# Performance work log

Hardware: AMD Instinct MI355X
Metric: run time of the kernel (lower is better)

The kernel has to match this reference:

```python
import jax, jax.numpy as jnp
import numpy as np

ANCHORS = jnp.array([[116.0, 90.0], [156.0, 198.0], [373.0, 326.0]], dtype=jnp.float32)
NUM_CLASSES = 80
IMG_SIZE = 416
EXP_CLAMP = 1000.0


def setup_inputs() -> dict:
    key = jax.random.key(0)
    # (batch, num_anchor*(num_classes+5), G, G) = (64, 255, 52, 52)
    X = jax.random.normal(key, (64, 255, 52, 52), dtype=jnp.float32)
    return {"X": X}


def reference(X):
    B = X.shape[0]
    G = X.shape[2]
    A = ANCHORS.shape[0]
    C = NUM_CLASSES
    ratio = IMG_SIZE / G  # stride

    # (B, A, 5+C, G, G) -> (B, A, G, G, 5+C)
    pred = X.reshape(B, A, C + 5, G, G).transpose(0, 1, 3, 4, 2)

    x = jax.nn.sigmoid(pred[..., 0])
    y = jax.nn.sigmoid(pred[..., 1])
    w = pred[..., 2]
    h = pred[..., 3]
    conf = jax.nn.sigmoid(pred[..., 4])
    clss = pred[..., 5:]  # raw logits, matching the torch module

    grid = jnp.arange(G, dtype=jnp.float32)
    coor_x = grid.reshape(1, 1, 1, G)   # varies along last (column) axis
    coor_y = grid.reshape(1, 1, G, 1)   # varies along row axis

    scale_anchors = ANCHORS / ratio
    anchor_x = scale_anchors[:, 0].reshape(1, A, 1, 1)
    anchor_y = scale_anchors[:, 1].reshape(1, A, 1, 1)

    bx = x + coor_x
    by = y + coor_y
    bw = jnp.minimum(jnp.exp(w), EXP_CLAMP) * anchor_x
    bh = jnp.minimum(jnp.exp(h), EXP_CLAMP) * anchor_y
    pred_boxes = jnp.stack([bx, by, bw, bh], axis=-1)  # (B, A, G, G, 4)

    output = jnp.concatenate(
        [
            pred_boxes.reshape(B, -1, 4) * ratio,
            conf.reshape(B, -1, 1),
            clss.reshape(B, -1, C),
        ],
        axis=-1,
    )  # (B, A*G*G, 5+C)
    return output
```

## Files before the change

kernel.cpp:

```cpp
#include <hip/hip_runtime.h>
#include <math.h>


constexpr int G   = 52;
constexpr int GG  = G * G;
constexpr int NA  = 3;
constexpr int NC  = 85;
constexpr int RPW = 16;
constexpr int WTB = GG / RPW;
constexpr float RATIO = 8.0f;

typedef float f32x4 __attribute__((ext_vector_type(4)));

__device__ __forceinline__ float sigmoidf_(float v) {
    return 1.0f / (1.0f + expf(-v));
}

__global__ __launch_bounds__(256)
void yolo_head_kernel(const float* __restrict__ X, float* __restrict__ out,
                      int total_wt) {
    __shared__ float lds[4 * RPW * NC];

    const int w    = threadIdx.x >> 6;
    const int lane = threadIdx.x & 63;
    const int t    = blockIdx.x * 4 + w;
    if (t >= total_wt) return;

    const int ba  = t / WTB;
    const int rem = t - ba * WTB;
    const int ij0 = rem * RPW;

    const int a = ba % NA;
    const float ax = (a == 0) ? 116.0f : ((a == 1) ? 156.0f : 373.0f);
    const float ay = (a == 0) ?  90.0f : ((a == 1) ? 198.0f : 326.0f);

    const f32x4* src = reinterpret_cast<const f32x4*>(X)
                       + (size_t)ba * NC * (GG / 4) + (ij0 >> 2);
    float* ldsw = lds + w * (RPW * NC);

    const int c0 = lane >> 2;
    const int v4 = lane & 3;
    const int jl = v4 << 2;

    #pragma unroll
    for (int it = 0; it < 6; ++it) {
        if (it < 5 || lane < 20) {
            const int c = it * 16 + c0;
            f32x4 val = src[(size_t)c * (GG / 4) + v4];
            if (it == 0 && lane < 20) {
                #pragma unroll
                for (int m = 0; m < 4; ++m) {
                    const int ij = ij0 + jl + m;
                    const float v = val[m];
                    float r;
                    if (c == 0)      r = (sigmoidf_(v) + (float)(ij % G)) * RATIO;
                    else if (c == 1) r = (sigmoidf_(v) + (float)(ij / G)) * RATIO;
                    else if (c == 2) r = fminf(expf(v), 1000.0f) * ax;
                    else if (c == 3) r = fminf(expf(v), 1000.0f) * ay;
                    else             r = sigmoidf_(v);
                    ldsw[(jl + m) * NC + c] = r;
                }
            } else {
                #pragma unroll
                for (int m = 0; m < 4; ++m)
                    ldsw[(jl + m) * NC + c] = val[m];
            }
        }
    }

    asm volatile("" ::: "memory");

    const f32x4* lds4 = reinterpret_cast<const f32x4*>(ldsw);
    f32x4* dst4 = reinterpret_cast<f32x4*>(out)
                  + (size_t)ba * (GG * NC / 4) + (size_t)rem * (RPW * NC / 4);
    #pragma unroll
    for (int it = 0; it < 6; ++it) {
        const int idx = it * 64 + lane;
        if (it < 5 || lane < 20) {
            __builtin_nontemporal_store(lds4[idx], &dst4[idx]);
        }
    }
}

extern "C" void kernel_launch(void* const* d_in, const int* in_sizes, int n_in,
                              void* d_out, int out_size, void* d_ws, size_t ws_size,
                              hipStream_t stream) {
    const float* X = (const float*)d_in[0];
    float* out = (float*)d_out;
    const int B = in_sizes[0] / (NA * NC * GG);
    const int total_wt = B * NA * WTB;
    const int blocks = (total_wt + 3) / 4;
    yolo_head_kernel<<<dim3((unsigned)blocks), dim3(256), 0, stream>>>(X, out, total_wt);
}
```

Baseline: 64.75 us.

## Convert to persistent grid-stride waves with register double-buffered tile prefetch

Replaces the one-tile-per-wave launch with a fixed grid of 1792 blocks, where each wave loops over tiles with a stride of the total wave count. The next tile's global loads go into a second register set while the current tile is transposed through LDS and stored, so load latency overlaps with store work. Launch bounds now request 7 blocks per CU. The cost is doubled register use for the prefetch buffers, and the fixed grid size may not match the CU count well.

```diff
diff --git a/kernel.cpp b/kernel.cpp
--- a/kernel.cpp
+++ b/kernel.cpp
@@ -16,69 +16,97 @@
     return 1.0f / (1.0f + expf(-v));
 }
 
-__global__ __launch_bounds__(256)
+__global__ __launch_bounds__(256, 7)
 void yolo_head_kernel(const float* __restrict__ X, float* __restrict__ out,
-                      int total_wt) {
+                      int total_wt, int nwaves) {
     __shared__ float lds[4 * RPW * NC];
 
     const int w    = threadIdx.x >> 6;
     const int lane = threadIdx.x & 63;
-    const int t    = blockIdx.x * 4 + w;
+    const int c0   = lane >> 2;
+    const int v4   = lane & 3;
+    const int jl   = v4 << 2;
+
+    float* ldsw = lds + w * (RPW * NC);
+    const f32x4* lds4 = reinterpret_cast<const f32x4*>(ldsw);
+
+    f32x4 A[6], B[6];
+
+    auto load_tile = [&](f32x4* R, int tt) {
+        const int ba  = tt / WTB;
+        const int rem = tt - ba * WTB;
+        const f32x4* src = reinterpret_cast<const f32x4*>(X)
+            + (size_t)ba * NC * (GG / 4) + (size_t)(rem * 4) + v4;
+        #pragma unroll
+        for (int it = 0; it < 6; ++it) {
+            if (it < 5 || lane < 20) {
+                R[it] = src[(size_t)(it * 16 + c0) * (GG / 4)];
+            }
+        }
+    };
+
+    auto process_tile = [&](f32x4* R, int tt) {
+        const int ba  = tt / WTB;
+        const int rem = tt - ba * WTB;
+        const int ij0 = rem * RPW;
+        const int a   = ba % NA;
+        const float ax = (a == 0) ? 116.0f : ((a == 1) ? 156.0f : 373.0f);
+        const float ay = (a == 0) ?  90.0f : ((a == 1) ? 198.0f : 326.0f);
+
+        #pragma unroll
+        for (int it = 0; it < 6; ++it) {
+            const int c = it * 16 + c0;
+            if (it == 0) {
+                if (lane < 20) {
+                    #pragma unroll
+                    for (int m = 0; m < 4; ++m) {
+                        const int ij = ij0 + jl + m;
+                        const float v = R[0][m];
+                        float r;
+                        if (c == 0)      r = (sigmoidf_(v) + (float)(ij % G)) * RATIO;
+                        else if (c == 1) r = (sigmoidf_(v) + (float)(ij / G)) * RATIO;
+                        else if (c == 2) r = fminf(expf(v), 1000.0f) * ax;
+                        else if (c == 3) r = fminf(expf(v), 1000.0f) * ay;
+                        else             r = sigmoidf_(v);
+                        ldsw[(jl + m) * NC + c] = r;
+                    }
+                } else {
+                    #pragma unroll
+                    for (int m = 0; m < 4; ++m)
+                        ldsw[(jl + m) * NC + c] = R[0][m];
+                }
+            } else if (it < 5 || lane < 20) {
+                #pragma unroll
+                for (int m = 0; m < 4; ++m)
+                    ldsw[(jl + m) * NC + c] = R[it][m];
+            }
+        }
+
+        asm volatile("" ::: "memory");
+
+        f32x4* dst4 = reinterpret_cast<f32x4*>(out) + (size_t)tt * (RPW * NC / 4);
+        #pragma unroll
+        for (int it = 0; it < 6; ++it) {
+            const int idx = it * 64 + lane;
+            if (it < 5 || lane < 20) {
+                __builtin_nontemporal_store(lds4[idx], &dst4[idx]);
+            }
+        }
+    };
+
+    int t = blockIdx.x * 4 + w;
     if (t >= total_wt) return;
 
-    const int ba  = t / WTB;
-    const int rem = t - ba * WTB;
-    const int ij0 = rem * RPW;
-
-    const int a = ba % NA;
-    const float ax = (a == 0) ? 116.0f : ((a == 1) ? 156.0f : 373.0f);
-    const float ay = (a == 0) ?  90.0f : ((a == 1) ? 198.0f : 326.0f);
-
-    const f32x4* src = reinterpret_cast<const f32x4*>(X)
-                       + (size_t)ba * NC * (GG / 4) + (ij0 >> 2);
-    float* ldsw = lds + w * (RPW * NC);
-
-    const int c0 = lane >> 2;
-    const int v4 = lane & 3;
-    const int jl = v4 << 2;
-
-    #pragma unroll
-    for (int it = 0; it < 6; ++it) {
-        if (it < 5 || lane < 20) {
-            const int c = it * 16 + c0;
-            f32x4 val = src[(size_t)c * (GG / 4) + v4];
-            if (it == 0 && lane < 20) {
-                #pragma unroll
-                for (int m = 0; m < 4; ++m) {
-                    const int ij = ij0 + jl + m;
-                    const float v = val[m];
-                    float r;
-                    if (c == 0)      r = (sigmoidf_(v) + (float)(ij % G)) * RATIO;
-                    else if (c == 1) r = (sigmoidf_(v) + (float)(ij / G)) * RATIO;
-                    else if (c == 2) r = fminf(expf(v), 1000.0f) * ax;
-                    else if (c == 3) r = fminf(expf(v), 1000.0f) * ay;
-                    else             r = sigmoidf_(v);
-                    ldsw[(jl + m) * NC + c] = r;
-                }
-            } else {
-                #pragma unroll
-                for (int m = 0; m < 4; ++m)
-                    ldsw[(jl + m) * NC + c] = val[m];
-            }
-        }
-    }
-
-    asm volatile("" ::: "memory");
-
-    const f32x4* lds4 = reinterpret_cast<const f32x4*>(ldsw);
-    f32x4* dst4 = reinterpret_cast<f32x4*>(out)
-                  + (size_t)ba * (GG * NC / 4) + (size_t)rem * (RPW * NC / 4);
-    #pragma unroll
-    for (int it = 0; it < 6; ++it) {
-        const int idx = it * 64 + lane;
-        if (it < 5 || lane < 20) {
-            __builtin_nontemporal_store(lds4[idx], &dst4[idx]);
-        }
+    load_tile(A, t);
+    while (true) {
+        const int tn = t + nwaves;
+        const bool has_next = (tn < total_wt);
+        if (has_next) load_tile(B, tn);
+        process_tile(A, t);
+        if (!has_next) break;
+        t = tn;
+        #pragma unroll
+        for (int i = 0; i < 6; ++i) A[i] = B[i];
     }
 }
 
@@ -89,6 +117,8 @@
     float* out = (float*)d_out;
     const int B = in_sizes[0] / (NA * NC * GG);
     const int total_wt = B * NA * WTB;
-    const int blocks = (total_wt + 3) / 4;
-    yolo_head_kernel<<<dim3((unsigned)blocks), dim3(256), 0, stream>>>(X, out, total_wt);
+    const int blocks = 1792;
+    const int nwaves = blocks * 4;
+    yolo_head_kernel<<<dim3((unsigned)blocks), dim3(256), 0, stream>>>(
+        X, out, total_wt, nwaves);
 }
```

Result: slower. 71.72 us (+10.8%).
